# Kernel optimization log

Hardware: AMD Instinct MI355X
Metric: run time of the kernel (lower is better)

The kernel has to match this reference:

```python
import jax, jax.numpy as jnp
import numpy as np

BLOCK = 32          # MX block size along the last (contraction) dim
E4M3_MAX = 448.0    # max representable magnitude of float8_e4m3fn
E4M3_MAX_POW2 = 8.0 # floor(log2(448))


def mx_quant_dequant(x):
    """Emulate torchao MXTensor.to_mx: per-32-block shared E8M0 scale + fp8 e4m3 cast,
    then dequantize back to fp32 (what torch.matmul on MXTensor computes with)."""
    orig_shape = x.shape
    xb = x.reshape(orig_shape[:-1] + (orig_shape[-1] // BLOCK, BLOCK))
    amax = jnp.max(jnp.abs(xb), axis=-1, keepdims=True)
    safe_amax = jnp.where(amax == 0, 1.0, amax)
    # shared power-of-two exponent: floor(log2(amax)) - max_pow2(e4m3)
    shared_exp = jnp.floor(jnp.log2(safe_amax)) - E4M3_MAX_POW2
    scale = jnp.exp2(jnp.clip(shared_exp, -127.0, 127.0))  # E8M0 range
    q = jnp.clip(xb / scale, -E4M3_MAX, E4M3_MAX).astype(jnp.float8_e4m3fn)
    return (q.astype(x.dtype) * scale).reshape(orig_shape)


def setup_inputs() -> dict:
    key = jax.random.key(0)
    k1, k2, k3 = jax.random.split(key, 3)
    M = K = N = 4096
    return {
        "x_mx": jax.random.normal(k1, (M, K), dtype=jnp.float32),
        "mat1": jax.random.normal(k2, (K, K), dtype=jnp.float32),
        "mat2": jax.random.normal(k3, (K, N), dtype=jnp.float32),
    }


def reference(x_mx, mat1, mat2):
    # inputs arrive as MX tensors in the original -> quantize/dequantize them first
    xq = mx_quant_dequant(x_mx)
    m1q = mx_quant_dequant(mat1)
    m2q = mx_quant_dequant(mat2)
    x_high = xq @ m1q                       # [M, K] fp32 matmul of dequantized MX
    x_requant = mx_quant_dequant(x_high)    # re-quantize intermediate to MX fp8
    out = x_requant @ m2q                   # [M, N]
    return out
```

## Files before the change

### kernel.cpp

```cpp
#include <hip/hip_runtime.h>
#include <cstdint>

typedef unsigned short u16;
typedef __bf16 bf16x8 __attribute__((ext_vector_type(8)));
typedef float f32x4 __attribute__((ext_vector_type(4)));
typedef float f32x2 __attribute__((ext_vector_type(2)));

#define AS1 __attribute__((address_space(1)))
#define AS3 __attribute__((address_space(3)))


__device__ __forceinline__ int floor_log2(float x) {
    unsigned b = __float_as_uint(x);
    if (b < 0x00800000u) {
        b = __float_as_uint(x * 16777216.0f);
        return (int)(b >> 23) - 151;
    }
    return (int)(b >> 23) - 127;
}

__device__ __forceinline__ float exp2i(int e) {
    if (e >= -126) return __uint_as_float((unsigned)(e + 127) << 23);
    return __uint_as_float(0x00400000u >> (-127 - e));
}

__device__ __forceinline__ int shared_exp(float amax) {
    float safe = (amax == 0.0f) ? 1.0f : amax;
    int se = floor_log2(safe) - 8;
    return se < -127 ? -127 : (se > 127 ? 127 : se);
}

__device__ __forceinline__ void qdq2s(float v0, float v1, float i0, float i1,
                                      float s0, float s1, float& o0, float& o1) {
    float y0 = fminf(fmaxf(v0 * i0, -448.0f), 448.0f);
    float y1 = fminf(fmaxf(v1 * i1, -448.0f), 448.0f);
    int pk = __builtin_amdgcn_cvt_pk_fp8_f32(y0, y1, 0, false);
    f32x2 f = __builtin_amdgcn_cvt_pk_f32_fp8(pk, false);
    o0 = f.x * s0;
    o1 = f.y * s1;
}

__device__ __forceinline__ unsigned pack_bf16(float a, float b) {
    return (__float_as_uint(a) >> 16) | (__float_as_uint(b) & 0xffff0000u);
}

__global__ void qdq_rows(const float* __restrict__ in, u16* __restrict__ out) {
    size_t t = (size_t)blockIdx.x * 256 + threadIdx.x;
    float4 v0 = ((const float4*)in)[t * 2];
    float4 v1 = ((const float4*)in)[t * 2 + 1];
    float a = fmaxf(fmaxf(fabsf(v0.x), fabsf(v0.y)), fmaxf(fabsf(v0.z), fabsf(v0.w)));
    a = fmaxf(a, fmaxf(fmaxf(fabsf(v1.x), fabsf(v1.y)), fmaxf(fabsf(v1.z), fabsf(v1.w))));
    a = fmaxf(a, __shfl_xor(a, 1));
    a = fmaxf(a, __shfl_xor(a, 2));
    int se = shared_exp(a);
    float s = exp2i(se), inv = exp2i(-se);
    float q0, q1, q2, q3, q4, q5, q6, q7;
    qdq2s(v0.x, v0.y, inv, inv, s, s, q0, q1);
    qdq2s(v0.z, v0.w, inv, inv, s, s, q2, q3);
    qdq2s(v1.x, v1.y, inv, inv, s, s, q4, q5);
    qdq2s(v1.z, v1.w, inv, inv, s, s, q6, q7);
    uint4 o;
    o.x = pack_bf16(q0, q1);
    o.y = pack_bf16(q2, q3);
    o.z = pack_bf16(q4, q5);
    o.w = pack_bf16(q6, q7);
    ((uint4*)out)[t] = o;
}

__global__ void qdq_transpose(const float* __restrict__ in, u16* __restrict__ out,
                              int R, int C) {
    __shared__ u16 tile[64][70];
    int c0 = blockIdx.x * 64, r0 = blockIdx.y * 64;
    int t = threadIdx.x;
    #pragma unroll
    for (int p = 0; p < 4; ++p) {
        int lin = p * 256 + t;
        int row = lin >> 4;
        int c4  = lin & 15;
        float4 v = *(const float4*)(in + (size_t)(r0 + row) * C + c0 + c4 * 4);
        float a = fmaxf(fmaxf(fabsf(v.x), fabsf(v.y)), fmaxf(fabsf(v.z), fabsf(v.w)));
        a = fmaxf(a, __shfl_xor(a, 1));
        a = fmaxf(a, __shfl_xor(a, 2));
        a = fmaxf(a, __shfl_xor(a, 4));
        int se = shared_exp(a);
        float s = exp2i(se), inv = exp2i(-se);
        float q0, q1, q2, q3;
        qdq2s(v.x, v.y, inv, inv, s, s, q0, q1);
        qdq2s(v.z, v.w, inv, inv, s, s, q2, q3);
        tile[c4 * 4 + 0][row] = (u16)(__float_as_uint(q0) >> 16);
        tile[c4 * 4 + 1][row] = (u16)(__float_as_uint(q1) >> 16);
        tile[c4 * 4 + 2][row] = (u16)(__float_as_uint(q2) >> 16);
        tile[c4 * 4 + 3][row] = (u16)(__float_as_uint(q3) >> 16);
    }
    __syncthreads();
    #pragma unroll
    for (int p = 0; p < 4; ++p) {
        int lin = p * 256 + t;
        int n  = lin >> 4;
        int k4 = lin & 15;
        unsigned lo = *(const unsigned*)&tile[n][k4 * 4];
        unsigned hi = *(const unsigned*)&tile[n][k4 * 4 + 2];
        *(uint2*)(out + (size_t)(c0 + n) * R + r0 + k4 * 4) = make_uint2(lo, hi);
    }
}

__device__ __forceinline__ void gemm_core256(const u16* __restrict__ A,
                                             const u16* __restrict__ B,
                                             u16* As, u16* Bs,
                                             int m0, int n0, f32x4 acc[8][4]) {
    const int K = 4096;
    const int t = threadIdx.x;
    const int w = t >> 6, lane = t & 63;
    const int l15 = lane & 15, lq = lane >> 4, fr = l15 & 7;
    const int wmc = (w >> 2) * 64;
    const int wnc = (w & 3) * 32;

    int aoff[4][2], boff[2][2];
    #pragma unroll
    for (int m = 0; m < 4; ++m)
        #pragma unroll
        for (int ks = 0; ks < 2; ++ks)
            aoff[m][ks] = (wmc + m * 16 + l15) * 64 + (((ks * 4 + lq) ^ fr) * 8);
    #pragma unroll
    for (int nf = 0; nf < 2; ++nf)
        #pragma unroll
        for (int ks = 0; ks < 2; ++ks)
            boff[nf][ks] = (wnc + nf * 16 + l15) * 64 + (((ks * 4 + lq) ^ fr) * 8);

    const int ch0 = t, ch1 = 512 + t;
    const int r0 = ch0 >> 3, r1 = ch1 >> 3;
    const size_t soff0 = (size_t)r0 * K + ((ch0 & 7) ^ (r0 & 7)) * 8;
    const size_t soff1 = (size_t)r1 * K + ((ch1 & 7) ^ (r1 & 7)) * 8;
    const int doff0 = ch0 * 8, doff1 = ch1 * 8;

    const u16* pA0 = A + (size_t)m0 * K;
    const u16* pA1 = A + (size_t)(m0 + 128) * K;
    const u16* pB0 = B + (size_t)n0 * K;
    const u16* pB1 = B + (size_t)(n0 + 128) * K;

    u16* A0b0 = As;            u16* A1b0 = As + 8192;
    u16* A0b1 = As + 16384;    u16* A1b1 = As + 24576;
    u16* B0b0 = Bs;            u16* B1b0 = Bs + 8192;
    u16* B0b1 = Bs + 16384;    u16* B1b1 = Bs + 24576;

#define STAGE(dst, src, kt) do {                                                          \
    __builtin_amdgcn_global_load_lds((const AS1 unsigned*)((src) + soff0 + (size_t)(kt) * 64), \
                                     (AS3 unsigned*)&(dst)[doff0], 16, 0, 0);             \
    __builtin_amdgcn_global_load_lds((const AS1 unsigned*)((src) + soff1 + (size_t)(kt) * 64), \
                                     (AS3 unsigned*)&(dst)[doff1], 16, 0, 0); } while (0)

#define LOAD_A(base) do {                                                                 \
    _Pragma("unroll") for (int m = 0; m < 4; ++m)                                         \
    _Pragma("unroll") for (int ks = 0; ks < 2; ++ks)                                      \
        af[m][ks] = *(const bf16x8*)&(base)[aoff[m][ks]]; } while (0)

#define LOAD_B(dstf, base) do {                                                           \
    _Pragma("unroll") for (int nf = 0; nf < 2; ++nf)                                      \
    _Pragma("unroll") for (int ks = 0; ks < 2; ++ks)                                      \
        dstf[nf][ks] = *(const bf16x8*)&(base)[boff[nf][ks]]; } while (0)

#define MFMA_Q(mb, nb, BF) do {                                                           \
    _Pragma("unroll") for (int m = 0; m < 4; ++m)                                         \
    _Pragma("unroll") for (int nf = 0; nf < 2; ++nf)                                      \
    _Pragma("unroll") for (int ks = 0; ks < 2; ++ks)                                      \
        acc[(mb) + m][(nb) + nf] = __builtin_amdgcn_mfma_f32_16x16x32_bf16(               \
            af[m][ks], BF[nf][ks], acc[(mb) + m][(nb) + nf], 0, 0, 0); } while (0)

#define MID() do { __builtin_amdgcn_s_barrier();                                          \
    asm volatile("s_waitcnt lgkmcnt(0)" ::: "memory");                                    \
    __builtin_amdgcn_s_setprio(1); } while (0)
#define END() do { __builtin_amdgcn_s_setprio(0); __builtin_amdgcn_s_barrier(); } while (0)
#define VMW() asm volatile("s_waitcnt vmcnt(6)" ::: "memory")

    #pragma unroll
    for (int mi = 0; mi < 8; ++mi)
        #pragma unroll
        for (int ni = 0; ni < 4; ++ni)
            acc[mi][ni] = (f32x4)0.f;

    bf16x8 af[4][2], bf0[2][2], bf1[2][2];

    STAGE(A0b0, pA0, 0);
    STAGE(B1b0, pB1, 0);
    STAGE(A1b0, pA1, 0);
    STAGE(B0b0, pB0, 0);
    STAGE(A0b1, pA0, 1);
    STAGE(B1b1, pB1, 1);
    STAGE(A1b1, pA1, 1);
    VMW();
    __builtin_amdgcn_s_barrier();

    #pragma unroll 1
    for (int i = 0; i < 32; ++i) {
        const int t1 = (2 * i + 1) & 63, t2 = (2 * i + 2) & 63, t3 = (2 * i + 3) & 63;
        LOAD_A(A0b0); LOAD_B(bf0, B0b0);
        STAGE(B0b1, pB0, t1);
        MID(); MFMA_Q(0, 0, bf0); END();
        LOAD_B(bf1, B1b0);
        STAGE(A0b0, pA0, t2);
        MID(); MFMA_Q(0, 2, bf1); END();
        LOAD_A(A1b0);
        STAGE(B1b0, pB1, t2);
        MID(); MFMA_Q(4, 2, bf1); END();
        STAGE(A1b0, pA1, t2);
        VMW();
        MID(); MFMA_Q(4, 0, bf0); END();
        LOAD_A(A0b1); LOAD_B(bf0, B0b1);
        STAGE(B0b0, pB0, t2);
        MID(); MFMA_Q(0, 0, bf0); END();
        LOAD_B(bf1, B1b1);
        STAGE(A0b1, pA0, t3);
        MID(); MFMA_Q(0, 2, bf1); END();
        LOAD_A(A1b1);
        STAGE(B1b1, pB1, t3);
        MID(); MFMA_Q(4, 2, bf1); END();
        STAGE(A1b1, pA1, t3);
        VMW();
        MID(); MFMA_Q(4, 0, bf0); END();
    }
#undef STAGE
#undef LOAD_A
#undef LOAD_B
#undef MFMA_Q
#undef MID
#undef END
#undef VMW
}

__global__ __launch_bounds__(512, 2) void gemm1_fused(const u16* __restrict__ A,
                                                      const u16* __restrict__ B,
                                                      u16* __restrict__ Cq) {
    const int N = 4096;
    extern __shared__ __align__(16) char smem[];
    u16* As = (u16*)smem;
    u16* Bs = (u16*)(smem + 65536);
    int m0 = blockIdx.y * 256, n0 = blockIdx.x * 256;
    f32x4 acc[8][4];
    gemm_core256(A, B, As, Bs, m0, n0, acc);

    const int t = threadIdx.x, w = t >> 6, lane = t & 63;
    const int l15 = lane & 15, lq = lane >> 4;
    const int wmc = (w >> 2) * 64, wnc = (w & 3) * 32;

    #pragma unroll
    for (int mi = 0; mi < 8; ++mi) {
        const int gr_base = m0 + (mi >> 2) * 128 + wmc + (mi & 3) * 16 + lq * 4;
        #pragma unroll
        for (int nq = 0; nq < 2; ++nq) {
            const int gc = n0 + nq * 128 + wnc + l15;
            float sc[4], iv[4];
            #pragma unroll
            for (int reg = 0; reg < 4; ++reg) {
                float a = fmaxf(fabsf(acc[mi][2 * nq][reg]), fabsf(acc[mi][2 * nq + 1][reg]));
                a = fmaxf(a, __shfl_xor(a, 1));
                a = fmaxf(a, __shfl_xor(a, 2));
                a = fmaxf(a, __shfl_xor(a, 4));
                a = fmaxf(a, __shfl_xor(a, 8));
                int se = shared_exp(a);
                sc[reg] = exp2i(se);
                iv[reg] = exp2i(-se);
            }
            #pragma unroll
            for (int reg = 0; reg < 4; ++reg) {
                float q0, q1;
                qdq2s(acc[mi][2 * nq][reg], acc[mi][2 * nq + 1][reg],
                      iv[reg], iv[reg], sc[reg], sc[reg], q0, q1);
                Cq[(size_t)(gr_base + reg) * N + gc]      = (u16)(__float_as_uint(q0) >> 16);
                Cq[(size_t)(gr_base + reg) * N + gc + 16] = (u16)(__float_as_uint(q1) >> 16);
            }
        }
    }
}

__global__ __launch_bounds__(512, 2) void gemm2(const u16* __restrict__ A,
                                                const u16* __restrict__ B,
                                                float* __restrict__ C) {
    const int N = 4096;
    extern __shared__ __align__(16) char smem[];
    u16* As = (u16*)smem;
    u16* Bs = (u16*)(smem + 65536);
    int m0 = blockIdx.y * 256, n0 = blockIdx.x * 256;
    f32x4 acc[8][4];
    gemm_core256(A, B, As, Bs, m0, n0, acc);

    const int t = threadIdx.x, w = t >> 6, lane = t & 63;
    const int l15 = lane & 15, lq = lane >> 4;
    const int wmc = (w >> 2) * 64, wnc = (w & 3) * 32;

    #pragma unroll
    for (int mi = 0; mi < 8; ++mi) {
        const int gr_base = m0 + (mi >> 2) * 128 + wmc + (mi & 3) * 16 + lq * 4;
        #pragma unroll
        for (int ni = 0; ni < 4; ++ni) {
            const int gc = n0 + (ni >> 1) * 128 + wnc + (ni & 1) * 16 + l15;
            #pragma unroll
            for (int reg = 0; reg < 4; ++reg)
                C[(size_t)(gr_base + reg) * N + gc] = acc[mi][ni][reg];
        }
    }
}

extern "C" void kernel_launch(void* const* d_in, const int* in_sizes, int n_in,
                              void* d_out, int out_size, void* d_ws, size_t ws_size,
                              hipStream_t stream) {
    const float* x  = (const float*)d_in[0];
    const float* m1 = (const float*)d_in[1];
    const float* m2 = (const float*)d_in[2];
    float* out = (float*)d_out;

    const int M = 4096, K = 4096, N = 4096;
    const size_t MB = 1024 * 1024;
    char* ws = (char*)d_ws;
    u16* xq   = (u16*)(ws + 0 * MB);
    u16* m1qT = (u16*)(ws + 32 * MB);
    u16* m2qT = (u16*)(ws + 64 * MB);
    u16* xrq  = (u16*)(ws + 96 * MB);

    static bool s_init = false;
    if (!s_init) {
        hipFuncSetAttribute((const void*)gemm1_fused,
                            hipFuncAttributeMaxDynamicSharedMemorySize, 131072);
        hipFuncSetAttribute((const void*)gemm2,
                            hipFuncAttributeMaxDynamicSharedMemorySize, 131072);
        s_init = true;
    }

    dim3 b(256);
    qdq_rows<<<dim3((M * K) / 2048), b, 0, stream>>>(x, xq);
    qdq_transpose<<<dim3(K / 64, K / 64), b, 0, stream>>>(m1, m1qT, K, K);
    qdq_transpose<<<dim3(N / 64, K / 64), b, 0, stream>>>(m2, m2qT, K, N);
    gemm1_fused<<<dim3(N / 256, M / 256), dim3(512), 131072, stream>>>(xq, m1qT, xrq);
    gemm2<<<dim3(N / 256, M / 256), dim3(512), 131072, stream>>>(xrq, m2qT, out);
}
```

Baseline: 425.2 us.

## Overlap LDS fragment loads with MFMAs and swizzle workgroup tile mapping

```diff
diff --git a/kernel.cpp b/kernel.cpp
--- a/kernel.cpp
+++ b/kernel.cpp
@@ -160,9 +160,9 @@
         dstf[nf][ks] = *(const bf16x8*)&(base)[boff[nf][ks]]; } while (0)
 
 #define MFMA_Q(mb, nb, BF) do {                                                           \
+    _Pragma("unroll") for (int ks = 0; ks < 2; ++ks)                                      \
     _Pragma("unroll") for (int m = 0; m < 4; ++m)                                         \
     _Pragma("unroll") for (int nf = 0; nf < 2; ++nf)                                      \
-    _Pragma("unroll") for (int ks = 0; ks < 2; ++ks)                                      \
         acc[(mb) + m][(nb) + nf] = __builtin_amdgcn_mfma_f32_16x16x32_bf16(               \
             af[m][ks], BF[nf][ks], acc[(mb) + m][(nb) + nf], 0, 0, 0); } while (0)
 
@@ -189,34 +189,29 @@
     STAGE(A1b1, pA1, 1);
     VMW();
     __builtin_amdgcn_s_barrier();
+    LOAD_A(A0b0); LOAD_B(bf0, B0b0);
 
     #pragma unroll 1
     for (int i = 0; i < 32; ++i) {
         const int t1 = (2 * i + 1) & 63, t2 = (2 * i + 2) & 63, t3 = (2 * i + 3) & 63;
-        LOAD_A(A0b0); LOAD_B(bf0, B0b0);
         STAGE(B0b1, pB0, t1);
-        MID(); MFMA_Q(0, 0, bf0); END();
-        LOAD_B(bf1, B1b0);
+        MID(); MFMA_Q(0, 0, bf0); LOAD_B(bf1, B1b0); END();
         STAGE(A0b0, pA0, t2);
-        MID(); MFMA_Q(0, 2, bf1); END();
-        LOAD_A(A1b0);
+        MID(); MFMA_Q(0, 2, bf1); LOAD_A(A1b0); END();
         STAGE(B1b0, pB1, t2);
         MID(); MFMA_Q(4, 2, bf1); END();
         STAGE(A1b0, pA1, t2);
         VMW();
-        MID(); MFMA_Q(4, 0, bf0); END();
-        LOAD_A(A0b1); LOAD_B(bf0, B0b1);
+        MID(); MFMA_Q(4, 0, bf0); LOAD_A(A0b1); LOAD_B(bf0, B0b1); END();
         STAGE(B0b0, pB0, t2);
-        MID(); MFMA_Q(0, 0, bf0); END();
-        LOAD_B(bf1, B1b1);
+        MID(); MFMA_Q(0, 0, bf0); LOAD_B(bf1, B1b1); END();
         STAGE(A0b1, pA0, t3);
-        MID(); MFMA_Q(0, 2, bf1); END();
-        LOAD_A(A1b1);
+        MID(); MFMA_Q(0, 2, bf1); LOAD_A(A1b1); END();
         STAGE(B1b1, pB1, t3);
         MID(); MFMA_Q(4, 2, bf1); END();
         STAGE(A1b1, pA1, t3);
         VMW();
-        MID(); MFMA_Q(4, 0, bf0); END();
+        MID(); MFMA_Q(4, 0, bf0); LOAD_A(A0b0); LOAD_B(bf0, B0b0); END();
     }
 #undef STAGE
 #undef LOAD_A
@@ -227,6 +222,13 @@
 #undef VMW
 }
 
+__device__ __forceinline__ void swizzle_bid(int& m0, int& n0) {
+    int id = blockIdx.x;
+    int wg = (id & 7) * 32 + (id >> 3);
+    m0 = (wg >> 4) * 256;
+    n0 = (wg & 15) * 256;
+}
+
 __global__ __launch_bounds__(512, 2) void gemm1_fused(const u16* __restrict__ A,
                                                       const u16* __restrict__ B,
                                                       u16* __restrict__ Cq) {
@@ -234,7 +236,8 @@
     extern __shared__ __align__(16) char smem[];
     u16* As = (u16*)smem;
     u16* Bs = (u16*)(smem + 65536);
-    int m0 = blockIdx.y * 256, n0 = blockIdx.x * 256;
+    int m0, n0;
+    swizzle_bid(m0, n0);
     f32x4 acc[8][4];
     gemm_core256(A, B, As, Bs, m0, n0, acc);
 
@@ -279,7 +282,8 @@
     extern __shared__ __align__(16) char smem[];
     u16* As = (u16*)smem;
     u16* Bs = (u16*)(smem + 65536);
-    int m0 = blockIdx.y * 256, n0 = blockIdx.x * 256;
+    int m0, n0;
+    swizzle_bid(m0, n0);
     f32x4 acc[8][4];
     gemm_core256(A, B, As, Bs, m0, n0, acc);
 
@@ -329,6 +333,6 @@
     qdq_rows<<<dim3((M * K) / 2048), b, 0, stream>>>(x, xq);
     qdq_transpose<<<dim3(K / 64, K / 64), b, 0, stream>>>(m1, m1qT, K, K);
     qdq_transpose<<<dim3(N / 64, K / 64), b, 0, stream>>>(m2, m2qT, K, N);
-    gemm1_fused<<<dim3(N / 256, M / 256), dim3(512), 131072, stream>>>(xq, m1qT, xrq);
-    gemm2<<<dim3(N / 256, M / 256), dim3(512), 131072, stream>>>(xrq, m2qT, out);
-}
+    gemm1_fused<<<dim3(256), dim3(512), 131072, stream>>>(xq, m1qT, xrq);
+    gemm2<<<dim3(256), dim3(512), 131072, stream>>>(xrq, m2qT, out);
+}
```

Result: no change. 426.3 us (+0.3%).
